# Optimization experiments

Measured on AMD Instinct MI355X. Metric: run time of the kernel, lower is better.

## Reference

```python
import jax, jax.numpy as jnp
import numpy as np
from jax import lax

GATE_SLOPE = 10.0
ALPHA = 0.8
B, IN_DIM, OUT_DIM, NUM_BASIS = 256, 128, 128, 16


def setup_inputs() -> dict:
    key = jax.random.key(0)
    k1, k2, k3, k4, k5, k6 = jax.random.split(key, 6)
    pshape = (IN_DIM, OUT_DIM, NUM_BASIS)
    return {
        "x": jax.random.normal(k1, (B, IN_DIM), dtype=jnp.float32),
        "k": jax.random.uniform(k2, pshape, dtype=jnp.float32) * 2.0 + 0.5,
        "Ec": jax.random.uniform(k3, pshape, dtype=jnp.float32) * 2.0 + 0.5,
        "Ps": jax.random.uniform(k4, pshape, dtype=jnp.float32) * 1.5 + 0.5,
        "bias": jax.random.normal(k5, pshape, dtype=jnp.float32) * 0.1,
        "coef": jax.random.normal(k6, pshape, dtype=jnp.float32),
    }


def reference(x, k, Ec, Ps, bias, coef):
    # Sequential hysteresis over the batch dimension (lax.scan replaces the
    # per-sample Python loop). Carry: (prev_x, branch_sign), each [in,out,nb].
    pshape = k.shape  # (in_dim, out_dim, num_basis)

    def step(carry, xb):
        prev_x, bs = carry
        xs = xb[:, None, None]                       # [in,1,1] broadcasts to pshape
        dx = xs - prev_x
        is_up = jax.nn.sigmoid(GATE_SLOPE * dx)
        crossed_pos = jax.nn.sigmoid(GATE_SLOPE * (xs - Ec))
        crossed_neg = jax.nn.sigmoid(GATE_SLOPE * (-xs - Ec))
        su = is_up * crossed_pos
        sl = (1.0 - is_up) * crossed_neg
        target = su - sl + (1.0 - su - sl) * bs
        bs_new = ALPHA * bs + (1.0 - ALPHA) * target
        basis = Ps * jnp.tanh(k * (xs + Ec * bs_new)) + bias
        # torch does prev_x.copy_(x_sample.detach()) -> stop_gradient
        prev_x_new = lax.stop_gradient(jnp.broadcast_to(xs, pshape))
        return (prev_x_new, bs_new), basis

    init = (jnp.zeros(pshape, x.dtype), jnp.ones(pshape, x.dtype))
    _, basis_all = lax.scan(step, init, x)            # [B,in,out,nb]
    # weighted sum over in_dim and num_basis -> [B, out_dim]
    output = jnp.einsum('bion,ion->bo', basis_all, coef)
    return output
```

## Files before the change

### kernel.cpp

```cpp
#include <hip/hip_runtime.h>

#define GATE_SLOPE 10.0f
#define ALPHA 0.8f
constexpr int B_ = 256, IN_DIM = 128, OUT_DIM = 128, NB = 16;

__device__ __forceinline__ float rcpf(float x)  { return __builtin_amdgcn_rcpf(x); }
__device__ __forceinline__ float ex2f(float x)  { return __builtin_amdgcn_exp2f(x); }

template<int CTRL>
__device__ __forceinline__ float dpp_add(float v) {
    int s = __builtin_amdgcn_update_dpp(0, __builtin_bit_cast(int, v),
                                        CTRL, 0xF, 0xF, true);
    return v + __builtin_bit_cast(float, s);
}

__launch_bounds__(256, 4)
__global__ void ferro_kernel(const float* __restrict__ x,
                             const float* __restrict__ k,
                             const float* __restrict__ Ec,
                             const float* __restrict__ Ps,
                             const float* __restrict__ bias,
                             const float* __restrict__ coef,
                             float* __restrict__ out)
{
    constexpr float LOG2E = 1.4426950408889634f;
    constexpr float S = GATE_SLOPE * LOG2E;

    __shared__ float2 xsup[B_];

    const int t   = threadIdx.x;
    const int blk = blockIdx.x;
    const int i      = blk >> 3;
    const int o_base = (blk & 7) << 4;

    {
        float xb = x[t * IN_DIM + i];
        float xp = (t == 0) ? 0.0f : x[(t - 1) * IN_DIM + i];
        float up = rcpf(1.0f + ex2f((xp - xb) * S));
        xsup[t] = make_float2(xb, up);
    }
    __syncthreads();

    const long pidx = (long)i * (OUT_DIM * NB) + (long)o_base * NB + t;
    const float kk = k[pidx];
    const float ec = Ec[pidx];
    const float ps = Ps[pidx];
    const float bi = bias[pidx];
    const float cf = coef[pidx];

    const int o = o_base + (t >> 4);
    const int n = t & 15;

    const float ecS = ec * S;
    const float E2c = ex2f(2.0f * ecS);
    const float kt  = kk * (2.0f * LOG2E);

    float bs = 1.0f;

    #pragma unroll 8
    for (int b = 0; b < B_; ++b) {
        const float2 xu = xsup[b];
        const float xs = xu.x;
        const float up = xu.y;

        float a1 = __builtin_fmaf(-xs, S, ecS);
        a1 = fminf(fmaxf(a1, -126.0f), 126.0f);
        const float e1 = ex2f(a1);
        const float cp = rcpf(1.0f + e1);
        const float cn = e1 * rcpf(e1 + E2c);

        const float su = up * cp;
        const float sl = __builtin_fmaf(-up, cn, cn);
        const float d  = su - sl;
        const float m  = (1.0f - su) - sl;
        const float tgt = __builtin_fmaf(m, bs, d);
        bs = __builtin_fmaf(1.0f - ALPHA, tgt, ALPHA * bs);

        const float z  = __builtin_fmaf(ec, bs, xs);
        const float e3 = ex2f(kt * z);
        const float th = __builtin_fmaf(-2.0f, rcpf(1.0f + e3), 1.0f);
        const float basis = __builtin_fmaf(ps, th, bi);

        float v = basis * cf;
        v = dpp_add<0xB1>(v);
        v = dpp_add<0x4E>(v);
        v = dpp_add<0x141>(v);
        v = dpp_add<0x140>(v);
        if (n == 0) atomicAdd(&out[b * OUT_DIM + o], v);
    }
}

extern "C" void kernel_launch(void* const* d_in, const int* in_sizes, int n_in,
                              void* d_out, int out_size, void* d_ws, size_t ws_size,
                              hipStream_t stream) {
    const float* x    = (const float*)d_in[0];
    const float* k    = (const float*)d_in[1];
    const float* Ec   = (const float*)d_in[2];
    const float* Ps   = (const float*)d_in[3];
    const float* bias = (const float*)d_in[4];
    const float* coef = (const float*)d_in[5];
    float* out = (float*)d_out;

    hipMemsetAsync(out, 0, (size_t)out_size * sizeof(float), stream);

    dim3 grid(IN_DIM * 8);
    dim3 block(256);
    ferro_kernel<<<grid, block, 0, stream>>>(x, k, Ec, Ps, bias, coef, out);
}
```

Baseline: 153.0 us.

## Replicate atomic output buffers across workspace and restructure scan into two phases

Atomic adds now go to up to 32 replicated output buffers in the workspace, chosen by input index, and a second reduce kernel sums them into the output. This cuts atomic contention on each output element. The batch loop is also split into 8-step chunks: the gate math that does not depend on the carried state is computed first for the whole chunk, then the serial recurrence runs, which gives the scheduler more independent work per chunk. The cost is an extra memset over the replicas, an extra kernel launch, and more registers.

```diff
diff --git a/kernel.cpp b/kernel.cpp
--- a/kernel.cpp
+++ b/kernel.cpp
@@ -21,7 +21,8 @@
                              const float* __restrict__ Ps,
                              const float* __restrict__ bias,
                              const float* __restrict__ coef,
-                             float* __restrict__ out)
+                             float* __restrict__ target,
+                             int repmask)
 {
     constexpr float LOG2E = 1.4426950408889634f;
     constexpr float S = GATE_SLOPE * LOG2E;
@@ -55,39 +56,53 @@
     const float E2c = ex2f(2.0f * ecS);
     const float kt  = kk * (2.0f * LOG2E);
 
+    float* __restrict__ rbase = target + ((long)(i & repmask) << 15);
+
     float bs = 1.0f;
 
-    #pragma unroll 8
-    for (int b = 0; b < B_; ++b) {
-        const float2 xu = xsup[b];
-        const float xs = xu.x;
-        const float up = xu.y;
+    for (int b0 = 0; b0 < B_; b0 += 8) {
+        float dd[8], mm[8], xx[8];
+        #pragma unroll
+        for (int u = 0; u < 8; ++u) {
+            const float2 xu = xsup[b0 + u];
+            const float xs = xu.x;
+            const float up = xu.y;
+            float a1 = __builtin_fmaf(-xs, S, ecS);
+            a1 = fminf(fmaxf(a1, -126.0f), 126.0f);
+            const float e1 = ex2f(a1);
+            const float cp = rcpf(1.0f + e1);
+            const float cn = e1 * rcpf(e1 + E2c);
+            const float su = up * cp;
+            const float sl = __builtin_fmaf(-up, cn, cn);
+            dd[u] = su - sl;
+            mm[u] = (1.0f - su) - sl;
+            xx[u] = xs;
+        }
+        #pragma unroll
+        for (int u = 0; u < 8; ++u) {
+            const float tgt = __builtin_fmaf(mm[u], bs, dd[u]);
+            bs = __builtin_fmaf(1.0f - ALPHA, tgt, ALPHA * bs);
+            const float z  = __builtin_fmaf(ec, bs, xx[u]);
+            const float e3 = ex2f(kt * z);
+            const float th = __builtin_fmaf(-2.0f, rcpf(1.0f + e3), 1.0f);
+            const float basis = __builtin_fmaf(ps, th, bi);
+            float v = basis * cf;
+            v = dpp_add<0xB1>(v);
+            v = dpp_add<0x4E>(v);
+            v = dpp_add<0x141>(v);
+            v = dpp_add<0x140>(v);
+            if (n == 0) atomicAdd(&rbase[((b0 + u) << 7) + o], v);
+        }
+    }
+}
 
-        float a1 = __builtin_fmaf(-xs, S, ecS);
-        a1 = fminf(fmaxf(a1, -126.0f), 126.0f);
-        const float e1 = ex2f(a1);
-        const float cp = rcpf(1.0f + e1);
-        const float cn = e1 * rcpf(e1 + E2c);
-
-        const float su = up * cp;
-        const float sl = __builtin_fmaf(-up, cn, cn);
-        const float d  = su - sl;
-        const float m  = (1.0f - su) - sl;
-        const float tgt = __builtin_fmaf(m, bs, d);
-        bs = __builtin_fmaf(1.0f - ALPHA, tgt, ALPHA * bs);
-
-        const float z  = __builtin_fmaf(ec, bs, xs);
-        const float e3 = ex2f(kt * z);
-        const float th = __builtin_fmaf(-2.0f, rcpf(1.0f + e3), 1.0f);
-        const float basis = __builtin_fmaf(ps, th, bi);
-
-        float v = basis * cf;
-        v = dpp_add<0xB1>(v);
-        v = dpp_add<0x4E>(v);
-        v = dpp_add<0x141>(v);
-        v = dpp_add<0x140>(v);
-        if (n == 0) atomicAdd(&out[b * OUT_DIM + o], v);
-    }
+__global__ void reduce_kernel(const float* __restrict__ ws,
+                              float* __restrict__ out, int R)
+{
+    const int j = blockIdx.x * blockDim.x + threadIdx.x;
+    float s = 0.0f;
+    for (int r = 0; r < R; ++r) s += ws[((long)r << 15) + j];
+    out[j] = s;
 }
 
 extern "C" void kernel_launch(void* const* d_in, const int* in_sizes, int n_in,
@@ -100,10 +115,23 @@
     const float* bias = (const float*)d_in[4];
     const float* coef = (const float*)d_in[5];
     float* out = (float*)d_out;
+    float* ws  = (float*)d_ws;
 
-    hipMemsetAsync(out, 0, (size_t)out_size * sizeof(float), stream);
+    const size_t repBytes = (size_t)32768 * sizeof(float);
+    int R = 0;
+    if (ws_size >= repBytes) {
+        R = 1;
+        while (R < 32 && (size_t)(R * 2) * repBytes <= ws_size) R <<= 1;
+    }
 
-    dim3 grid(IN_DIM * 8);
-    dim3 block(256);
-    ferro_kernel<<<grid, block, 0, stream>>>(x, k, Ec, Ps, bias, coef, out);
+    if (R >= 2) {
+        hipMemsetAsync(ws, 0, (size_t)R * repBytes, stream);
+        ferro_kernel<<<dim3(IN_DIM * 8), dim3(256), 0, stream>>>(
+            x, k, Ec, Ps, bias, coef, ws, R - 1);
+        reduce_kernel<<<dim3(128), dim3(256), 0, stream>>>(ws, out, R);
+    } else {
+        hipMemsetAsync(out, 0, (size_t)out_size * sizeof(float), stream);
+        ferro_kernel<<<dim3(IN_DIM * 8), dim3(256), 0, stream>>>(
+            x, k, Ec, Ps, bias, coef, out, 0);
+    }
 }
```

New measurement: 140.3 us. -8.3%, faster.
